# Optimization experiments

Measured on AMD Instinct MI355X. Metric: run time of the kernel, lower is better.

The kernel has to match this reference:

```python
import jax, jax.numpy as jnp
import numpy as np

B, LS, LT = 32, 64, 64
V_SRC, V_TGT = 32000, 32000
E, H = 512, 512


def setup_inputs() -> dict:
    key = jax.random.key(0)
    ks = jax.random.split(key, 16)
    s = 0.05
    inp = {
        "src": jax.random.randint(ks[0], (B, LS), 0, V_SRC),
        "tgt": jax.random.randint(ks[1], (B, LT), 0, V_TGT),
        # encoder params
        "enc_embed": jax.random.normal(ks[2], (V_SRC, E), jnp.float32) * s,
        "enc_wih": jax.random.normal(ks[3], (E, H), jnp.float32) * s,
        "enc_bih": jax.random.normal(ks[4], (H,), jnp.float32) * s,
        "enc_whh": jax.random.normal(ks[5], (H, H), jnp.float32) * s,
        "enc_bhh": jax.random.normal(ks[6], (H,), jnp.float32) * s,
        # decoder params
        "dec_embed": jax.random.normal(ks[7], (V_TGT, E), jnp.float32) * s,
        "dec_wih": jax.random.normal(ks[8], (E, H), jnp.float32) * s,
        "dec_bih": jax.random.normal(ks[9], (H,), jnp.float32) * s,
        "dec_whh": jax.random.normal(ks[10], (H, H), jnp.float32) * s,
        "dec_bhh": jax.random.normal(ks[11], (H,), jnp.float32) * s,
        "h2o_w": jax.random.normal(ks[12], (H, V_TGT), jnp.float32) * s,
        "h2o_b": jax.random.normal(ks[13], (V_TGT,), jnp.float32) * s,
    }
    return inp


def _rnn_scan(tokens, embed, wih, bih, whh, bhh, h0):
    # tokens: (N, L) int; returns (final hidden (N,H), all hiddens (L,N,H))
    xs = embed[tokens].transpose(1, 0, 2)  # (L, N, E)

    def step(h, x):
        h = jnp.tanh(x @ wih + bih + h @ whh + bhh)
        return h, h

    h_last, hs = jax.lax.scan(step, h0, xs)
    return h_last, hs


def reference(src, tgt, enc_embed, enc_wih, enc_bih, enc_whh, enc_bhh,
              dec_embed, dec_wih, dec_bih, dec_whh, dec_bhh, h2o_w, h2o_b):
    n = src.shape[0]
    h0 = jnp.zeros((n, enc_whh.shape[0]), dtype=enc_whh.dtype)
    # encoder: tanh RNN over src, keep only final hidden (teacher-forced training path)
    hidden, _ = _rnn_scan(src, enc_embed, enc_wih, enc_bih, enc_whh, enc_bhh, h0)
    # decoder: tanh RNN over tgt with teacher forcing
    _, dec_hs = _rnn_scan(tgt, dec_embed, dec_wih, dec_bih, dec_whh, dec_bhh, hidden)  # (Lt, N, H)
    # per-step h2o + LogSoftmax, batched over all steps at once (same math)
    logits = dec_hs @ h2o_w + h2o_b  # (Lt, N, V)
    outputs = jax.nn.log_softmax(logits, axis=-1).transpose(1, 0, 2)  # (N, Lt, V)
    return outputs
```

## Files before the change

### kernel.cpp

```cpp
#include <hip/hip_runtime.h>

#define Bd 32
#define Ld 64
#define Hd 512
#define Vd 32000

typedef __bf16 bf16_t;
typedef __bf16 bf16x8 __attribute__((ext_vector_type(8)));
typedef float  f32x4  __attribute__((ext_vector_type(4)));

#define HCHUNK 132
#define HIDX(e) ((((e) >> 7) * HCHUNK) + ((e) & 127))

__global__ void k_prep(
    const int* __restrict__ src, const int* __restrict__ tgt,
    const float* __restrict__ enc_embed, const float* __restrict__ enc_wih,
    const float* __restrict__ enc_bih, const float* __restrict__ enc_bhh,
    const float* __restrict__ dec_embed, const float* __restrict__ dec_wih,
    const float* __restrict__ dec_bih, const float* __restrict__ dec_bhh,
    float* __restrict__ Aenc, float* __restrict__ Adec,
    unsigned long long* __restrict__ encX, unsigned long long* __restrict__ decX)
{
    __shared__ float sm[16 * Hd];
    __shared__ int tokl[16];
    const int tid = threadIdx.x;
    const int bid = blockIdx.x;

    {
        unsigned wgi = ((unsigned)bid << 8) + tid;
        if (wgi < 32768) encX[wgi] = ~0ull;
        else             decX[wgi - 32768] = ~0ull;
    }
    const bool isDec = bid >= 128;
    const int rb = (isDec ? bid - 128 : bid) << 4;
    const int*   toks = isDec ? tgt : src;
    const float* emb  = isDec ? dec_embed : enc_embed;
    const float* wih  = isDec ? dec_wih : enc_wih;
    const float* bi   = isDec ? dec_bih : enc_bih;
    const float* bh   = isDec ? dec_bhh : enc_bhh;
    float*       A    = isDec ? Adec : Aenc;
    if (tid < 16) {
        int r = rb + tid;
        tokl[tid] = toks[(r & 31) * Ld + (r >> 5)];
    }
    __syncthreads();
    #pragma unroll
    for (int u = 0; u < 8; ++u) {
        int f = tid + (u << 8);
        int row = f >> 7, c4 = f & 127;
        ((float4*)sm)[f] = ((const float4*)(emb + (size_t)tokl[row] * Hd))[c4];
    }
    __syncthreads();
    const int j0 = tid, j1 = tid + 256;
    float acc0[16], acc1[16];
    #pragma unroll
    for (int r = 0; r < 16; ++r) { acc0[r] = 0.f; acc1[r] = 0.f; }
    #pragma unroll 4
    for (int k = 0; k < Hd; ++k) {
        float w0 = wih[(size_t)k * Hd + j0];
        float w1 = wih[(size_t)k * Hd + j1];
        #pragma unroll
        for (int r = 0; r < 16; ++r) {
            float x = sm[r * Hd + k];
            acc0[r] += x * w0;
            acc1[r] += x * w1;
        }
    }
    float bb0 = bi[j0] + bh[j0], bb1 = bi[j1] + bh[j1];
    #pragma unroll
    for (int r = 0; r < 16; ++r) {
        A[(size_t)(rb + r) * Hd + j0] = acc0[r] + bb0;
        A[(size_t)(rb + r) * Hd + j1] = acc1[r] + bb1;
    }
}

__global__ __launch_bounds__(256, 1) void k_rec(
    const float* __restrict__ enc_whh, const float* __restrict__ dec_whh,
    const float* __restrict__ Aenc, const float* __restrict__ Adec,
    unsigned long long* __restrict__ encX, unsigned long long* __restrict__ decX,
    bf16_t* __restrict__ dhsB,
    const float* __restrict__ w, bf16_t* __restrict__ wT)
{
    __shared__ float hl[2][4 * HCHUNK];
    __shared__ float ls[64][65];
    const int tid = threadIdx.x;
    const int bid = blockIdx.x;

    if (bid >= 256) {
        const int b2 = bid - 256;
        const int v0 = (b2 % 500) << 6;
        const int k0 = (b2 / 500) << 6;
        #pragma unroll
        for (int u = 0; u < 16; ++u) {
            int f = tid + (u << 8);
            int r = f >> 6, cc = f & 63;
            ls[r][cc] = w[(size_t)(k0 + r) * Vd + v0 + cc];
        }
        __syncthreads();
        #pragma unroll
        for (int u = 0; u < 16; ++u) {
            int f = tid + (u << 8);
            int vr = f >> 6, kk = f & 63;
            wT[(size_t)(v0 + vr) * Hd + k0 + kk] = (bf16_t)ls[kk][vr];
        }
        return;
    }

    const int c = bid & 31, p = bid >> 5;
    const int q = tid >> 6, lane = tid & 63;
    const int l4 = lane & 15, g = lane >> 4;
    const int jb = p << 6;
    const int col = jb + (q << 4) + l4;
    const int hw0 = HIDX(tid), hw1 = HIDX(tid + 256);

    {
        float wE[128];
        #pragma unroll
        for (int i = 0; i < 128; ++i) wE[i] = enc_whh[(size_t)((g << 7) + i) * Hd + col];
        for (int t = 0; t < Ld; ++t) {
            const int par = (t + 1) & 1;
            float aval = (lane < 16) ? Aenc[(size_t)(t * Bd + c) * Hd + col] : 0.f;
            if (t == 0) {
                hl[par][hw0] = 0.f; hl[par][hw1] = 0.f;
            } else {
                const unsigned long long* xs = encX + (size_t)(((t - 1) & 1) * Bd + c) * Hd;
                const unsigned want = (unsigned)(t - 1);
                unsigned long long v0 = __hip_atomic_load(xs + tid,       __ATOMIC_RELAXED, __HIP_MEMORY_SCOPE_AGENT);
                unsigned long long v1 = __hip_atomic_load(xs + tid + 256, __ATOMIC_RELAXED, __HIP_MEMORY_SCOPE_AGENT);
                while ((unsigned)(v0 >> 32) != want || (unsigned)(v1 >> 32) != want) {
                    __builtin_amdgcn_s_sleep(1);
                    if ((unsigned)(v0 >> 32) != want)
                        v0 = __hip_atomic_load(xs + tid,       __ATOMIC_RELAXED, __HIP_MEMORY_SCOPE_AGENT);
                    if ((unsigned)(v1 >> 32) != want)
                        v1 = __hip_atomic_load(xs + tid + 256, __ATOMIC_RELAXED, __HIP_MEMORY_SCOPE_AGENT);
                }
                union { unsigned u; float f; } c0, c1;
                c0.u = (unsigned)v0; c1.u = (unsigned)v1;
                hl[par][hw0] = c0.f; hl[par][hw1] = c1.f;
            }
            __syncthreads();
            const float4* h4 = (const float4*)(hl[par] + g * HCHUNK);
            float acc = 0.f;
            #pragma unroll
            for (int i = 0; i < 32; ++i) {
                float4 hv = h4[i];
                acc += wE[4*i]*hv.x + wE[4*i+1]*hv.y + wE[4*i+2]*hv.z + wE[4*i+3]*hv.w;
            }
            acc += __shfl_xor(acc, 16, 64);
            acc += __shfl_xor(acc, 32, 64);
            if (lane < 16) {
                float h = tanhf(aval + acc);
                union { float f; unsigned u; } cv; cv.f = h;
                unsigned long long pv = ((unsigned long long)(unsigned)t << 32) | cv.u;
                __hip_atomic_store(encX + (size_t)((t & 1) * Bd + c) * Hd + col, pv,
                                   __ATOMIC_RELAXED, __HIP_MEMORY_SCOPE_AGENT);
            }
        }
    }
    {
        float wD[128];
        #pragma unroll
        for (int i = 0; i < 128; ++i) wD[i] = dec_whh[(size_t)((g << 7) + i) * Hd + col];
        for (int s = 0; s < Ld; ++s) {
            const int par = (s + 1) & 1;
            float aval = (lane < 16) ? Adec[(size_t)(s * Bd + c) * Hd + col] : 0.f;
            {
                const unsigned long long* xs = (s == 0)
                    ? (encX + (size_t)(((Ld - 1) & 1) * Bd + c) * Hd)
                    : (decX + (size_t)(((s - 1) & 1) * Bd + c) * Hd);
                const unsigned want = (s == 0) ? (unsigned)(Ld - 1) : (unsigned)(64 + s - 1);
                unsigned long long v0 = __hip_atomic_load(xs + tid,       __ATOMIC_RELAXED, __HIP_MEMORY_SCOPE_AGENT);
                unsigned long long v1 = __hip_atomic_load(xs + tid + 256, __ATOMIC_RELAXED, __HIP_MEMORY_SCOPE_AGENT);
                while ((unsigned)(v0 >> 32) != want || (unsigned)(v1 >> 32) != want) {
                    __builtin_amdgcn_s_sleep(1);
                    if ((unsigned)(v0 >> 32) != want)
                        v0 = __hip_atomic_load(xs + tid,       __ATOMIC_RELAXED, __HIP_MEMORY_SCOPE_AGENT);
                    if ((unsigned)(v1 >> 32) != want)
                        v1 = __hip_atomic_load(xs + tid + 256, __ATOMIC_RELAXED, __HIP_MEMORY_SCOPE_AGENT);
                }
                union { unsigned u; float f; } c0, c1;
                c0.u = (unsigned)v0; c1.u = (unsigned)v1;
                hl[par][hw0] = c0.f; hl[par][hw1] = c1.f;
            }
            __syncthreads();
            const float4* h4 = (const float4*)(hl[par] + g * HCHUNK);
            float acc = 0.f;
            #pragma unroll
            for (int i = 0; i < 32; ++i) {
                float4 hv = h4[i];
                acc += wD[4*i]*hv.x + wD[4*i+1]*hv.y + wD[4*i+2]*hv.z + wD[4*i+3]*hv.w;
            }
            acc += __shfl_xor(acc, 16, 64);
            acc += __shfl_xor(acc, 32, 64);
            if (lane < 16) {
                float h = tanhf(aval + acc);
                union { float f; unsigned u; } cv; cv.f = h;
                unsigned long long pv = ((unsigned long long)(unsigned)(64 + s) << 32) | cv.u;
                __hip_atomic_store(decX + (size_t)((s & 1) * Bd + c) * Hd + col, pv,
                                   __ATOMIC_RELAXED, __HIP_MEMORY_SCOPE_AGENT);
                dhsB[((size_t)c * Ld + s) * Hd + col] = (bf16_t)h;
            }
        }
    }
}

__global__ __launch_bounds__(256, 2) void k_gemm(
    const bf16_t* __restrict__ Amat, const bf16_t* __restrict__ Bmat,
    const float* __restrict__ bias, float* __restrict__ out,
    float2* __restrict__ part2)
{
    __shared__ bf16_t At[128 * 32];
    __shared__ bf16_t Bt[128 * 32];
    __shared__ float smM[128][2];
    __shared__ float smL[128][2];
    const int tid = threadIdx.x;
    const int bid = blockIdx.x;
    const int lin = (bid & 7) * 500 + (bid >> 3);
    const int n0 = (lin & 15) << 7;
    const int yv = lin >> 4;
    const int v0 = yv << 7;
    const int w = tid >> 6, lane = tid & 63;
    const int l15 = lane & 15, q8 = lane >> 4;
    const int moff = (w & 1) << 6, voff = (w >> 1) << 6;

    f32x4 acc[4][4];
    #pragma unroll
    for (int mi = 0; mi < 4; ++mi)
        #pragma unroll
        for (int vi = 0; vi < 4; ++vi)
            acc[mi][vi] = f32x4{0.f, 0.f, 0.f, 0.f};

    const int f0 = tid, f1 = tid + 256;
    const int row0 = f0 >> 2, sub0 = f0 & 3, sw0 = sub0 ^ (row0 & 3);
    const int row1 = f1 >> 2, sub1 = f1 & 3, sw1 = sub1 ^ (row1 & 3);
    const bf16_t* aP0 = Amat + (size_t)(n0 + row0) * Hd + (sub0 << 3);
    const bf16_t* aP1 = Amat + (size_t)(n0 + row1) * Hd + (sub1 << 3);
    const bf16_t* bP0 = Bmat + (size_t)(v0 + row0) * Hd + (sub0 << 3);
    const bf16_t* bP1 = Bmat + (size_t)(v0 + row1) * Hd + (sub1 << 3);

    uint4 pa0 = *(const uint4*)(aP0), pa1 = *(const uint4*)(aP1);
    uint4 pb0 = *(const uint4*)(bP0), pb1 = *(const uint4*)(bP1);

    for (int kb = 0; kb < 16; ++kb) {
        __syncthreads();
        *(uint4*)(At + row0 * 32 + (sw0 << 3)) = pa0;
        *(uint4*)(At + row1 * 32 + (sw1 << 3)) = pa1;
        *(uint4*)(Bt + row0 * 32 + (sw0 << 3)) = pb0;
        *(uint4*)(Bt + row1 * 32 + (sw1 << 3)) = pb1;
        __syncthreads();
        if (kb < 15) {
            int ko = (kb + 1) << 5;
            pa0 = *(const uint4*)(aP0 + ko); pa1 = *(const uint4*)(aP1 + ko);
            pb0 = *(const uint4*)(bP0 + ko); pb1 = *(const uint4*)(bP1 + ko);
        }
        bf16x8 af[4], bfr[4];
        #pragma unroll
        for (int mi = 0; mi < 4; ++mi) {
            int m = moff + (mi << 4) + l15;
            af[mi] = *(const bf16x8*)(At + m * 32 + (((q8 ^ (m & 3)) & 3) << 3));
        }
        #pragma unroll
        for (int vi = 0; vi < 4; ++vi) {
            int vv = voff + (vi << 4) + l15;
            bfr[vi] = *(const bf16x8*)(Bt + vv * 32 + (((q8 ^ (vv & 3)) & 3) << 3));
        }
        #pragma unroll
        for (int mi = 0; mi < 4; ++mi)
            #pragma unroll
            for (int vi = 0; vi < 4; ++vi)
                acc[mi][vi] = __builtin_amdgcn_mfma_f32_16x16x32_bf16(af[mi], bfr[vi], acc[mi][vi], 0, 0, 0);
    }

    float bz[4];
    #pragma unroll
    for (int vi = 0; vi < 4; ++vi) bz[vi] = bias[v0 + voff + (vi << 4) + l15];

    float rm[16], rl[16];
    #pragma unroll
    for (int k = 0; k < 16; ++k) rm[k] = -3.4e38f;
    #pragma unroll
    for (int mi = 0; mi < 4; ++mi)
        #pragma unroll
        for (int r = 0; r < 4; ++r)
            #pragma unroll
            for (int vi = 0; vi < 4; ++vi)
                rm[mi * 4 + r] = fmaxf(rm[mi * 4 + r], acc[mi][vi][r] + bz[vi]);
    #pragma unroll
    for (int mask = 1; mask < 16; mask <<= 1)
        #pragma unroll
        for (int k = 0; k < 16; ++k)
            rm[k] = fmaxf(rm[k], __shfl_xor(rm[k], mask, 64));
    #pragma unroll
    for (int k = 0; k < 16; ++k) rl[k] = 0.f;
    #pragma unroll
    for (int vi = 0; vi < 4; ++vi) {
        int col = v0 + voff + (vi << 4) + l15;
        #pragma unroll
        for (int mi = 0; mi < 4; ++mi) {
            int row = n0 + moff + (mi << 4) + (q8 << 2);
            #pragma unroll
            for (int r = 0; r < 4; ++r) {
                float z = acc[mi][vi][r] + bz[vi];
                out[(size_t)(row + r) * Vd + col] = z;
                rl[mi * 4 + r] += __expf(z - rm[mi * 4 + r]);
            }
        }
    }
    #pragma unroll
    for (int mask = 1; mask < 16; mask <<= 1)
        #pragma unroll
        for (int k = 0; k < 16; ++k)
            rl[k] += __shfl_xor(rl[k], mask, 64);

    if (l15 == 0) {
        int half = w >> 1;
        #pragma unroll
        for (int mi = 0; mi < 4; ++mi)
            #pragma unroll
            for (int r = 0; r < 4; ++r) {
                int rloc = moff + (mi << 4) + (q8 << 2) + r;
                smM[rloc][half] = rm[mi * 4 + r];
                smL[rloc][half] = rl[mi * 4 + r];
            }
    }
    __syncthreads();
    if (tid < 128) {
        float m0 = smM[tid][0], m1 = smM[tid][1];
        float l0 = smL[tid][0], l1 = smL[tid][1];
        float M = fmaxf(m0, m1);
        float L = l0 * __expf(m0 - M) + l1 * __expf(m1 - M);
        part2[(size_t)(n0 + tid) * 250 + yv] = make_float2(M, L);
    }
}

__global__ void k_lsub(float* __restrict__ out, const float2* __restrict__ part2)
{
    const int n = blockIdx.x, tid = threadIdx.x;
    __shared__ float smx[256], sl[256];
    float m = -3.4e38f, l = 0.f;
    if (tid < 250) {
        float2 pp = part2[(size_t)n * 250 + tid];
        m = pp.x; l = pp.y;
    }
    smx[tid] = m; sl[tid] = l;
    __syncthreads();
    for (int s2 = 128; s2 > 0; s2 >>= 1) {
        if (tid < s2) {
            float m1 = smx[tid], l1 = sl[tid];
            float m2 = smx[tid + s2], l2 = sl[tid + s2];
            float nm = fmaxf(m1, m2);
            sl[tid] = l1 * __expf(m1 - nm) + l2 * __expf(m2 - nm);
            smx[tid] = nm;
        }
        __syncthreads();
    }
    const float z = smx[0] + __logf(sl[0]);
    float4* row = (float4*)(out + (size_t)n * Vd);
    #pragma unroll 4
    for (int i = 0; i < 31; ++i) {
        int idx = i * 256 + tid;
        float4 x = row[idx];
        x.x -= z; x.y -= z; x.z -= z; x.w -= z;
        row[idx] = x;
    }
    if (tid < 64) {
        int idx = 7936 + tid;
        float4 x = row[idx];
        x.x -= z; x.y -= z; x.z -= z; x.w -= z;
        row[idx] = x;
    }
}

extern "C" void kernel_launch(void* const* d_in, const int* in_sizes, int n_in,
                              void* d_out, int out_size, void* d_ws, size_t ws_size,
                              hipStream_t stream)
{
    const int*   src       = (const int*)d_in[0];
    const int*   tgt       = (const int*)d_in[1];
    const float* enc_embed = (const float*)d_in[2];
    const float* enc_wih   = (const float*)d_in[3];
    const float* enc_bih   = (const float*)d_in[4];
    const float* enc_whh   = (const float*)d_in[5];
    const float* enc_bhh   = (const float*)d_in[6];
    const float* dec_embed = (const float*)d_in[7];
    const float* dec_wih   = (const float*)d_in[8];
    const float* dec_bih   = (const float*)d_in[9];
    const float* dec_whh   = (const float*)d_in[10];
    const float* dec_bhh   = (const float*)d_in[11];
    const float* h2o_w     = (const float*)d_in[12];
    const float* h2o_b     = (const float*)d_in[13];
    float* out = (float*)d_out;

    char* ws = (char*)d_ws;
    float*  Aenc  = (float*)(ws);
    float*  Adec  = (float*)(ws + ((size_t)4 << 20));
    unsigned long long* encX = (unsigned long long*)(ws + ((size_t)8 << 20));
    unsigned long long* decX = (unsigned long long*)(ws + ((size_t)8 << 20) + (256 << 10));
    bf16_t* dhsB  = (bf16_t*)(ws + ((size_t)9 << 20));
    bf16_t* wT    = (bf16_t*)(ws + ((size_t)12 << 20));
    float2* part2 = (float2*)(ws);

    k_prep<<<256, 256, 0, stream>>>(src, tgt,
        enc_embed, enc_wih, enc_bih, enc_bhh,
        dec_embed, dec_wih, dec_bih, dec_bhh, Aenc, Adec, encX, decX);
    k_rec<<<4256, 256, 0, stream>>>(enc_whh, dec_whh, Aenc, Adec,
        encX, decX, dhsB, h2o_w, wT);
    k_gemm<<<4000, 256, 0, stream>>>(dhsB, wT, h2o_b, out, part2);
    k_lsub<<<2048, 256, 0, stream>>>(out, part2);
}
```

Baseline: 869.4 us.

## Move weight transpose into prep kernel and use direct global-to-LDS loads in GEMM

New measurement: 851.4 us. 2.1% less time.

```diff
diff --git a/kernel.cpp b/kernel.cpp
--- a/kernel.cpp
+++ b/kernel.cpp
@@ -11,6 +11,14 @@
 
 #define HCHUNK 132
 #define HIDX(e) ((((e) >> 7) * HCHUNK) + ((e) & 127))
+
+__device__ __forceinline__ void gl_lds16(const bf16_t* g, bf16_t* l)
+{
+    __builtin_amdgcn_global_load_lds(
+        (const __attribute__((address_space(1))) void*)(uintptr_t)(g),
+        (__attribute__((address_space(3))) void*)(uint32_t)(uintptr_t)(l),
+        16, 0, 0);
+}
 
 __global__ void k_prep(
     const int* __restrict__ src, const int* __restrict__ tgt,
@@ -19,58 +27,80 @@
     const float* __restrict__ dec_embed, const float* __restrict__ dec_wih,
     const float* __restrict__ dec_bih, const float* __restrict__ dec_bhh,
     float* __restrict__ Aenc, float* __restrict__ Adec,
+    const float* __restrict__ w, bf16_t* __restrict__ wT,
     unsigned long long* __restrict__ encX, unsigned long long* __restrict__ decX)
 {
-    __shared__ float sm[16 * Hd];
-    __shared__ int tokl[16];
+    __shared__ __align__(16) char smraw[33024];
     const int tid = threadIdx.x;
     const int bid = blockIdx.x;
 
-    {
-        unsigned wgi = ((unsigned)bid << 8) + tid;
-        if (wgi < 32768) encX[wgi] = ~0ull;
-        else             decX[wgi - 32768] = ~0ull;
-    }
-    const bool isDec = bid >= 128;
-    const int rb = (isDec ? bid - 128 : bid) << 4;
-    const int*   toks = isDec ? tgt : src;
-    const float* emb  = isDec ? dec_embed : enc_embed;
-    const float* wih  = isDec ? dec_wih : enc_wih;
-    const float* bi   = isDec ? dec_bih : enc_bih;
-    const float* bh   = isDec ? dec_bhh : enc_bhh;
-    float*       A    = isDec ? Adec : Aenc;
-    if (tid < 16) {
-        int r = rb + tid;
-        tokl[tid] = toks[(r & 31) * Ld + (r >> 5)];
-    }
-    __syncthreads();
-    #pragma unroll
-    for (int u = 0; u < 8; ++u) {
-        int f = tid + (u << 8);
-        int row = f >> 7, c4 = f & 127;
-        ((float4*)sm)[f] = ((const float4*)(emb + (size_t)tokl[row] * Hd))[c4];
-    }
-    __syncthreads();
-    const int j0 = tid, j1 = tid + 256;
-    float acc0[16], acc1[16];
-    #pragma unroll
-    for (int r = 0; r < 16; ++r) { acc0[r] = 0.f; acc1[r] = 0.f; }
-    #pragma unroll 4
-    for (int k = 0; k < Hd; ++k) {
-        float w0 = wih[(size_t)k * Hd + j0];
-        float w1 = wih[(size_t)k * Hd + j1];
+    if (bid < 256) {
+        {
+            unsigned wgi = ((unsigned)bid << 8) + tid;
+            if (wgi < 32768) encX[wgi] = ~0ull;
+            else             decX[wgi - 32768] = ~0ull;
+        }
+        float* sm  = (float*)smraw;
+        int*  tokl = (int*)(smraw + 32768);
+        const bool isDec = bid >= 128;
+        const int rb = (isDec ? bid - 128 : bid) << 4;
+        const int*   toks = isDec ? tgt : src;
+        const float* emb  = isDec ? dec_embed : enc_embed;
+        const float* wih  = isDec ? dec_wih : enc_wih;
+        const float* bi   = isDec ? dec_bih : enc_bih;
+        const float* bh   = isDec ? dec_bhh : enc_bhh;
+        float*       A    = isDec ? Adec : Aenc;
+        if (tid < 16) {
+            int r = rb + tid;
+            tokl[tid] = toks[(r & 31) * Ld + (r >> 5)];
+        }
+        __syncthreads();
+        #pragma unroll
+        for (int u = 0; u < 8; ++u) {
+            int f = tid + (u << 8);
+            int row = f >> 7, c4 = f & 127;
+            ((float4*)sm)[f] = ((const float4*)(emb + (size_t)tokl[row] * Hd))[c4];
+        }
+        __syncthreads();
+        const int j0 = tid, j1 = tid + 256;
+        float acc0[16], acc1[16];
+        #pragma unroll
+        for (int r = 0; r < 16; ++r) { acc0[r] = 0.f; acc1[r] = 0.f; }
+        #pragma unroll 4
+        for (int k = 0; k < Hd; ++k) {
+            float w0 = wih[(size_t)k * Hd + j0];
+            float w1 = wih[(size_t)k * Hd + j1];
+            #pragma unroll
+            for (int r = 0; r < 16; ++r) {
+                float x = sm[r * Hd + k];
+                acc0[r] += x * w0;
+                acc1[r] += x * w1;
+            }
+        }
+        float bb0 = bi[j0] + bh[j0], bb1 = bi[j1] + bh[j1];
         #pragma unroll
         for (int r = 0; r < 16; ++r) {
-            float x = sm[r * Hd + k];
-            acc0[r] += x * w0;
-            acc1[r] += x * w1;
-        }
-    }
-    float bb0 = bi[j0] + bh[j0], bb1 = bi[j1] + bh[j1];
-    #pragma unroll
-    for (int r = 0; r < 16; ++r) {
-        A[(size_t)(rb + r) * Hd + j0] = acc0[r] + bb0;
-        A[(size_t)(rb + r) * Hd + j1] = acc1[r] + bb1;
+            A[(size_t)(rb + r) * Hd + j0] = acc0[r] + bb0;
+            A[(size_t)(rb + r) * Hd + j1] = acc1[r] + bb1;
+        }
+    } else {
+        float (*ls)[65] = (float(*)[65])smraw;
+        const int b2 = bid - 256;
+        const int v0 = (b2 % 500) << 6;
+        const int k0 = (b2 / 500) << 6;
+        #pragma unroll
+        for (int u = 0; u < 16; ++u) {
+            int f = tid + (u << 8);
+            int r = f >> 6, cc = f & 63;
+            ls[r][cc] = w[(size_t)(k0 + r) * Vd + v0 + cc];
+        }
+        __syncthreads();
+        #pragma unroll
+        for (int u = 0; u < 16; ++u) {
+            int f = tid + (u << 8);
+            int vr = f >> 6, kk = f & 63;
+            wT[(size_t)(v0 + vr) * Hd + k0 + kk] = (bf16_t)ls[kk][vr];
+        }
     }
 }
 
@@ -78,34 +108,11 @@
     const float* __restrict__ enc_whh, const float* __restrict__ dec_whh,
     const float* __restrict__ Aenc, const float* __restrict__ Adec,
     unsigned long long* __restrict__ encX, unsigned long long* __restrict__ decX,
-    bf16_t* __restrict__ dhsB,
-    const float* __restrict__ w, bf16_t* __restrict__ wT)
+    bf16_t* __restrict__ dhsB)
 {
     __shared__ float hl[2][4 * HCHUNK];
-    __shared__ float ls[64][65];
     const int tid = threadIdx.x;
     const int bid = blockIdx.x;
-
-    if (bid >= 256) {
-        const int b2 = bid - 256;
-        const int v0 = (b2 % 500) << 6;
-        const int k0 = (b2 / 500) << 6;
-        #pragma unroll
-        for (int u = 0; u < 16; ++u) {
-            int f = tid + (u << 8);
-            int r = f >> 6, cc = f & 63;
-            ls[r][cc] = w[(size_t)(k0 + r) * Vd + v0 + cc];
-        }
-        __syncthreads();
-        #pragma unroll
-        for (int u = 0; u < 16; ++u) {
-            int f = tid + (u << 8);
-            int vr = f >> 6, kk = f & 63;
-            wT[(size_t)(v0 + vr) * Hd + k0 + kk] = (bf16_t)ls[kk][vr];
-        }
-        return;
-    }
-
     const int c = bid & 31, p = bid >> 5;
     const int q = tid >> 6, lane = tid & 63;
     const int l4 = lane & 15, g = lane >> 4;
@@ -209,8 +216,8 @@
     const float* __restrict__ bias, float* __restrict__ out,
     float2* __restrict__ part2)
 {
-    __shared__ bf16_t At[128 * 32];
-    __shared__ bf16_t Bt[128 * 32];
+    __shared__ __align__(16) bf16_t At[128 * 32];
+    __shared__ __align__(16) bf16_t Bt[128 * 32];
     __shared__ float smM[128][2];
     __shared__ float smL[128][2];
     const int tid = threadIdx.x;
@@ -230,39 +237,37 @@
         for (int vi = 0; vi < 4; ++vi)
             acc[mi][vi] = f32x4{0.f, 0.f, 0.f, 0.f};
 
-    const int f0 = tid, f1 = tid + 256;
-    const int row0 = f0 >> 2, sub0 = f0 & 3, sw0 = sub0 ^ (row0 & 3);
-    const int row1 = f1 >> 2, sub1 = f1 & 3, sw1 = sub1 ^ (row1 & 3);
-    const bf16_t* aP0 = Amat + (size_t)(n0 + row0) * Hd + (sub0 << 3);
-    const bf16_t* aP1 = Amat + (size_t)(n0 + row1) * Hd + (sub1 << 3);
-    const bf16_t* bP0 = Bmat + (size_t)(v0 + row0) * Hd + (sub0 << 3);
-    const bf16_t* bP1 = Bmat + (size_t)(v0 + row1) * Hd + (sub1 << 3);
-
-    uint4 pa0 = *(const uint4*)(aP0), pa1 = *(const uint4*)(aP1);
-    uint4 pb0 = *(const uint4*)(bP0), pb1 = *(const uint4*)(bP1);
+    const int srow = lane >> 2;
+    const int scol = (lane & 3) << 3;
+    bf16_t* ldsA0 = At + ((w << 1) + 0) * 512;
+    bf16_t* ldsA1 = At + ((w << 1) + 1) * 512;
+    bf16_t* ldsB0 = Bt + ((w << 1) + 0) * 512;
+    bf16_t* ldsB1 = Bt + ((w << 1) + 1) * 512;
+    const int r0 = ((w << 1) + 0) * 16 + srow;
+    const int r1 = ((w << 1) + 1) * 16 + srow;
+    const bf16_t* aS0 = Amat + (size_t)(n0 + r0) * Hd + scol;
+    const bf16_t* aS1 = Amat + (size_t)(n0 + r1) * Hd + scol;
+    const bf16_t* bS0 = Bmat + (size_t)(v0 + r0) * Hd + scol;
+    const bf16_t* bS1 = Bmat + (size_t)(v0 + r1) * Hd + scol;
 
     for (int kb = 0; kb < 16; ++kb) {
         __syncthreads();
-        *(uint4*)(At + row0 * 32 + (sw0 << 3)) = pa0;
-        *(uint4*)(At + row1 * 32 + (sw1 << 3)) = pa1;
-        *(uint4*)(Bt + row0 * 32 + (sw0 << 3)) = pb0;
-        *(uint4*)(Bt + row1 * 32 + (sw1 << 3)) = pb1;
-        __syncthreads();
-        if (kb < 15) {
-            int ko = (kb + 1) << 5;
-            pa0 = *(const uint4*)(aP0 + ko); pa1 = *(const uint4*)(aP1 + ko);
-            pb0 = *(const uint4*)(bP0 + ko); pb1 = *(const uint4*)(bP1 + ko);
-        }
+        const int ko = kb << 5;
+        gl_lds16(aS0 + ko, ldsA0);
+        gl_lds16(aS1 + ko, ldsA1);
+        gl_lds16(bS0 + ko, ldsB0);
+        gl_lds16(bS1 + ko, ldsB1);
+        __syncthreads();
         bf16x8 af[4], bfr[4];
         #pragma unroll
         for (int mi = 0; mi < 4; ++mi) {
             int m = moff + (mi << 4) + l15;
-            af[mi] = *(const bf16x8*)(At + m * 32 + (((q8 ^ (m & 3)) & 3) << 3));
+            af[mi] = *(const bf16x8*)(At + m * 32 + (q8 << 3));
         }
         #pragma unroll
         for (int vi = 0; vi < 4; ++vi) {
             int vv = voff + (vi << 4) + l15;
-            bfr[vi] = *(const bf16x8*)(Bt + vv * 32 + (((q8 ^ (vv & 3)) & 3) << 3));
+            bfr[vi] = *(const bf16x8*)(Bt + vv * 32 + (q8 << 3));
         }
         #pragma unroll
         for (int mi = 0; mi < 4; ++mi)
@@ -400,11 +405,12 @@
     bf16_t* wT    = (bf16_t*)(ws + ((size_t)12 << 20));
     float2* part2 = (float2*)(ws);
 
-    k_prep<<<256, 256, 0, stream>>>(src, tgt,
+    k_prep<<<4256, 256, 0, stream>>>(src, tgt,
         enc_embed, enc_wih, enc_bih, enc_bhh,
-        dec_embed, dec_wih, dec_bih, dec_bhh, Aenc, Adec, encX, decX);
-    k_rec<<<4256, 256, 0, stream>>>(enc_whh, dec_whh, Aenc, Adec,
-        encX, decX, dhsB, h2o_w, wT);
+        dec_embed, dec_wih, dec_bih, dec_bhh, Aenc, Adec,
+        h2o_w, wT, encX, decX);
+    k_rec<<<256, 256, 0, stream>>>(enc_whh, dec_whh, Aenc, Adec,
+        encX, decX, dhsB);
     k_gemm<<<4000, 256, 0, stream>>>(dhsB, wT, h2o_b, out, part2);
     k_lsub<<<2048, 256, 0, stream>>>(out, part2);
 }
```

## Move h2o weight transpose into prep kernel and widen recurrence epilogue

Applied to the files above, without the earlier changes.

Measured after the change: 835.5 us. 1.04x faster.

```diff
diff --git a/kernel.cpp b/kernel.cpp
--- a/kernel.cpp
+++ b/kernel.cpp
@@ -11,6 +11,12 @@
 
 #define HCHUNK 132
 #define HIDX(e) ((((e) >> 7) * HCHUNK) + ((e) & 127))
+
+__device__ __forceinline__ float ftanh(float x)
+{
+    float e = __expf(2.f * x);
+    return 1.f - 2.f / (e + 1.f);
+}
 
 __global__ void k_prep(
     const int* __restrict__ src, const int* __restrict__ tgt,
@@ -19,58 +25,80 @@
     const float* __restrict__ dec_embed, const float* __restrict__ dec_wih,
     const float* __restrict__ dec_bih, const float* __restrict__ dec_bhh,
     float* __restrict__ Aenc, float* __restrict__ Adec,
+    const float* __restrict__ w, bf16_t* __restrict__ wT,
     unsigned long long* __restrict__ encX, unsigned long long* __restrict__ decX)
 {
-    __shared__ float sm[16 * Hd];
-    __shared__ int tokl[16];
+    __shared__ __align__(16) char smraw[33024];
     const int tid = threadIdx.x;
     const int bid = blockIdx.x;
 
-    {
-        unsigned wgi = ((unsigned)bid << 8) + tid;
-        if (wgi < 32768) encX[wgi] = ~0ull;
-        else             decX[wgi - 32768] = ~0ull;
-    }
-    const bool isDec = bid >= 128;
-    const int rb = (isDec ? bid - 128 : bid) << 4;
-    const int*   toks = isDec ? tgt : src;
-    const float* emb  = isDec ? dec_embed : enc_embed;
-    const float* wih  = isDec ? dec_wih : enc_wih;
-    const float* bi   = isDec ? dec_bih : enc_bih;
-    const float* bh   = isDec ? dec_bhh : enc_bhh;
-    float*       A    = isDec ? Adec : Aenc;
-    if (tid < 16) {
-        int r = rb + tid;
-        tokl[tid] = toks[(r & 31) * Ld + (r >> 5)];
-    }
-    __syncthreads();
-    #pragma unroll
-    for (int u = 0; u < 8; ++u) {
-        int f = tid + (u << 8);
-        int row = f >> 7, c4 = f & 127;
-        ((float4*)sm)[f] = ((const float4*)(emb + (size_t)tokl[row] * Hd))[c4];
-    }
-    __syncthreads();
-    const int j0 = tid, j1 = tid + 256;
-    float acc0[16], acc1[16];
-    #pragma unroll
-    for (int r = 0; r < 16; ++r) { acc0[r] = 0.f; acc1[r] = 0.f; }
-    #pragma unroll 4
-    for (int k = 0; k < Hd; ++k) {
-        float w0 = wih[(size_t)k * Hd + j0];
-        float w1 = wih[(size_t)k * Hd + j1];
+    if (bid < 256) {
+        {
+            unsigned wgi = ((unsigned)bid << 8) + tid;
+            if (wgi < 32768) encX[wgi] = ~0ull;
+            else             decX[wgi - 32768] = ~0ull;
+        }
+        float* sm  = (float*)smraw;
+        int*  tokl = (int*)(smraw + 32768);
+        const bool isDec = bid >= 128;
+        const int rb = (isDec ? bid - 128 : bid) << 4;
+        const int*   toks = isDec ? tgt : src;
+        const float* emb  = isDec ? dec_embed : enc_embed;
+        const float* wih  = isDec ? dec_wih : enc_wih;
+        const float* bi   = isDec ? dec_bih : enc_bih;
+        const float* bh   = isDec ? dec_bhh : enc_bhh;
+        float*       A    = isDec ? Adec : Aenc;
+        if (tid < 16) {
+            int r = rb + tid;
+            tokl[tid] = toks[(r & 31) * Ld + (r >> 5)];
+        }
+        __syncthreads();
+        #pragma unroll
+        for (int u = 0; u < 8; ++u) {
+            int f = tid + (u << 8);
+            int row = f >> 7, c4 = f & 127;
+            ((float4*)sm)[f] = ((const float4*)(emb + (size_t)tokl[row] * Hd))[c4];
+        }
+        __syncthreads();
+        const int j0 = tid, j1 = tid + 256;
+        float acc0[16], acc1[16];
+        #pragma unroll
+        for (int r = 0; r < 16; ++r) { acc0[r] = 0.f; acc1[r] = 0.f; }
+        #pragma unroll 4
+        for (int k = 0; k < Hd; ++k) {
+            float w0 = wih[(size_t)k * Hd + j0];
+            float w1 = wih[(size_t)k * Hd + j1];
+            #pragma unroll
+            for (int r = 0; r < 16; ++r) {
+                float x = sm[r * Hd + k];
+                acc0[r] += x * w0;
+                acc1[r] += x * w1;
+            }
+        }
+        float bb0 = bi[j0] + bh[j0], bb1 = bi[j1] + bh[j1];
         #pragma unroll
         for (int r = 0; r < 16; ++r) {
-            float x = sm[r * Hd + k];
-            acc0[r] += x * w0;
-            acc1[r] += x * w1;
-        }
-    }
-    float bb0 = bi[j0] + bh[j0], bb1 = bi[j1] + bh[j1];
-    #pragma unroll
-    for (int r = 0; r < 16; ++r) {
-        A[(size_t)(rb + r) * Hd + j0] = acc0[r] + bb0;
-        A[(size_t)(rb + r) * Hd + j1] = acc1[r] + bb1;
+            A[(size_t)(rb + r) * Hd + j0] = acc0[r] + bb0;
+            A[(size_t)(rb + r) * Hd + j1] = acc1[r] + bb1;
+        }
+    } else {
+        float (*ls)[65] = (float(*)[65])smraw;
+        const int b2 = bid - 256;
+        const int v0 = (b2 % 500) << 6;
+        const int k0 = (b2 / 500) << 6;
+        #pragma unroll
+        for (int u = 0; u < 16; ++u) {
+            int f = tid + (u << 8);
+            int r = f >> 6, cc = f & 63;
+            ls[r][cc] = w[(size_t)(k0 + r) * Vd + v0 + cc];
+        }
+        __syncthreads();
+        #pragma unroll
+        for (int u = 0; u < 16; ++u) {
+            int f = tid + (u << 8);
+            int vr = f >> 6, kk = f & 63;
+            wT[(size_t)(v0 + vr) * Hd + k0 + kk] = (bf16_t)ls[kk][vr];
+        }
     }
 }
 
@@ -78,34 +106,12 @@
     const float* __restrict__ enc_whh, const float* __restrict__ dec_whh,
     const float* __restrict__ Aenc, const float* __restrict__ Adec,
     unsigned long long* __restrict__ encX, unsigned long long* __restrict__ decX,
-    bf16_t* __restrict__ dhsB,
-    const float* __restrict__ w, bf16_t* __restrict__ wT)
+    bf16_t* __restrict__ dhsB)
 {
     __shared__ float hl[2][4 * HCHUNK];
-    __shared__ float ls[64][65];
+    __shared__ float res[64];
     const int tid = threadIdx.x;
     const int bid = blockIdx.x;
-
-    if (bid >= 256) {
-        const int b2 = bid - 256;
-        const int v0 = (b2 % 500) << 6;
-        const int k0 = (b2 / 500) << 6;
-        #pragma unroll
-        for (int u = 0; u < 16; ++u) {
-            int f = tid + (u << 8);
-            int r = f >> 6, cc = f & 63;
-            ls[r][cc] = w[(size_t)(k0 + r) * Vd + v0 + cc];
-        }
-        __syncthreads();
-        #pragma unroll
-        for (int u = 0; u < 16; ++u) {
-            int f = tid + (u << 8);
-            int vr = f >> 6, kk = f & 63;
-            wT[(size_t)(v0 + vr) * Hd + k0 + kk] = (bf16_t)ls[kk][vr];
-        }
-        return;
-    }
-
     const int c = bid & 31, p = bid >> 5;
     const int q = tid >> 6, lane = tid & 63;
     const int l4 = lane & 15, g = lane >> 4;
@@ -118,10 +124,10 @@
         #pragma unroll
         for (int i = 0; i < 128; ++i) wE[i] = enc_whh[(size_t)((g << 7) + i) * Hd + col];
         for (int t = 0; t < Ld; ++t) {
-            const int par = (t + 1) & 1;
-            float aval = (lane < 16) ? Aenc[(size_t)(t * Bd + c) * Hd + col] : 0.f;
+            const int ip = (t + 1) & 1;
+            float aval = (tid < 64) ? Aenc[(size_t)(t * Bd + c) * Hd + jb + tid] : 0.f;
             if (t == 0) {
-                hl[par][hw0] = 0.f; hl[par][hw1] = 0.f;
+                hl[ip][hw0] = 0.f; hl[ip][hw1] = 0.f;
             } else {
                 const unsigned long long* xs = encX + (size_t)(((t - 1) & 1) * Bd + c) * Hd;
                 const unsigned want = (unsigned)(t - 1);
@@ -136,10 +142,10 @@
                 }
                 union { unsigned u; float f; } c0, c1;
                 c0.u = (unsigned)v0; c1.u = (unsigned)v1;
-                hl[par][hw0] = c0.f; hl[par][hw1] = c1.f;
+                hl[ip][hw0] = c0.f; hl[ip][hw1] = c1.f;
             }
             __syncthreads();
-            const float4* h4 = (const float4*)(hl[par] + g * HCHUNK);
+            const float4* h4 = (const float4*)(hl[ip] + g * HCHUNK);
             float acc = 0.f;
             #pragma unroll
             for (int i = 0; i < 32; ++i) {
@@ -148,11 +154,13 @@
             }
             acc += __shfl_xor(acc, 16, 64);
             acc += __shfl_xor(acc, 32, 64);
-            if (lane < 16) {
-                float h = tanhf(aval + acc);
+            if (lane < 16) res[(q << 4) + l4] = acc;
+            __syncthreads();
+            if (tid < 64) {
+                float h = ftanh(aval + res[tid]);
                 union { float f; unsigned u; } cv; cv.f = h;
                 unsigned long long pv = ((unsigned long long)(unsigned)t << 32) | cv.u;
-                __hip_atomic_store(encX + (size_t)((t & 1) * Bd + c) * Hd + col, pv,
+                __hip_atomic_store(encX + (size_t)((t & 1) * Bd + c) * Hd + jb + tid, pv,
                                    __ATOMIC_RELAXED, __HIP_MEMORY_SCOPE_AGENT);
             }
         }
@@ -162,8 +170,8 @@
         #pragma unroll
         for (int i = 0; i < 128; ++i) wD[i] = dec_whh[(size_t)((g << 7) + i) * Hd + col];
         for (int s = 0; s < Ld; ++s) {
-            const int par = (s + 1) & 1;
-            float aval = (lane < 16) ? Adec[(size_t)(s * Bd + c) * Hd + col] : 0.f;
+            const int ip = (s + 1) & 1;
+            float aval = (tid < 64) ? Adec[(size_t)(s * Bd + c) * Hd + jb + tid] : 0.f;
             {
                 const unsigned long long* xs = (s == 0)
                     ? (encX + (size_t)(((Ld - 1) & 1) * Bd + c) * Hd)
@@ -180,10 +188,10 @@
                 }
                 union { unsigned u; float f; } c0, c1;
                 c0.u = (unsigned)v0; c1.u = (unsigned)v1;
-                hl[par][hw0] = c0.f; hl[par][hw1] = c1.f;
+                hl[ip][hw0] = c0.f; hl[ip][hw1] = c1.f;
             }
             __syncthreads();
-            const float4* h4 = (const float4*)(hl[par] + g * HCHUNK);
+            const float4* h4 = (const float4*)(hl[ip] + g * HCHUNK);
             float acc = 0.f;
             #pragma unroll
             for (int i = 0; i < 32; ++i) {
@@ -192,13 +200,15 @@
             }
             acc += __shfl_xor(acc, 16, 64);
             acc += __shfl_xor(acc, 32, 64);
-            if (lane < 16) {
-                float h = tanhf(aval + acc);
+            if (lane < 16) res[(q << 4) + l4] = acc;
+            __syncthreads();
+            if (tid < 64) {
+                float h = ftanh(aval + res[tid]);
                 union { float f; unsigned u; } cv; cv.f = h;
                 unsigned long long pv = ((unsigned long long)(unsigned)(64 + s) << 32) | cv.u;
-                __hip_atomic_store(decX + (size_t)((s & 1) * Bd + c) * Hd + col, pv,
+                __hip_atomic_store(decX + (size_t)((s & 1) * Bd + c) * Hd + jb + tid, pv,
                                    __ATOMIC_RELAXED, __HIP_MEMORY_SCOPE_AGENT);
-                dhsB[((size_t)c * Ld + s) * Hd + col] = (bf16_t)h;
+                dhsB[((size_t)c * Ld + s) * Hd + jb + tid] = (bf16_t)h;
             }
         }
     }
@@ -400,11 +410,12 @@
     bf16_t* wT    = (bf16_t*)(ws + ((size_t)12 << 20));
     float2* part2 = (float2*)(ws);
 
-    k_prep<<<256, 256, 0, stream>>>(src, tgt,
+    k_prep<<<4256, 256, 0, stream>>>(src, tgt,
         enc_embed, enc_wih, enc_bih, enc_bhh,
-        dec_embed, dec_wih, dec_bih, dec_bhh, Aenc, Adec, encX, decX);
-    k_rec<<<4256, 256, 0, stream>>>(enc_whh, dec_whh, Aenc, Adec,
-        encX, decX, dhsB, h2o_w, wT);
+        dec_embed, dec_wih, dec_bih, dec_bhh, Aenc, Adec,
+        h2o_w, wT, encX, decX);
+    k_rec<<<256, 256, 0, stream>>>(enc_whh, dec_whh, Aenc, Adec,
+        encX, decX, dhsB);
     k_gemm<<<4000, 256, 0, stream>>>(dhsB, wT, h2o_b, out, part2);
     k_lsub<<<2048, 256, 0, stream>>>(out, part2);
 }
```
